# Kernel optimization log

Hardware: AMD Instinct MI355X
Metric: run time of the kernel (lower is better)

The kernel has to match this reference:

```python
import jax, jax.numpy as jnp
import numpy as np

D_MODEL = 1024
N_HEADS = 16
D_K = D_MODEL // N_HEADS


def setup_inputs() -> dict:
    key = jax.random.key(0)
    ks = jax.random.split(key, 5)
    scale = 1.0 / np.sqrt(D_MODEL)
    return {
        "x": jax.random.normal(ks[0], (2, 2048, D_MODEL), dtype=jnp.float32),
        "W_q": jax.random.normal(ks[1], (D_MODEL, D_MODEL), dtype=jnp.float32) * scale,
        "W_k": jax.random.normal(ks[2], (D_MODEL, D_MODEL), dtype=jnp.float32) * scale,
        "W_v": jax.random.normal(ks[3], (D_MODEL, D_MODEL), dtype=jnp.float32) * scale,
        "W_o": jax.random.normal(ks[4], (D_MODEL, D_MODEL), dtype=jnp.float32) * scale,
    }


def reference(x, W_q, W_k, W_v, W_o):
    # Weights are nn.Linear-style [out, in]; Linear(x) = x @ W.T
    B, T, _ = x.shape
    def split_heads(t):  # [B,T,D] -> [B,H,T,d_k]
        return t.reshape(B, T, N_HEADS, D_K).transpose(0, 2, 1, 3)
    Q = split_heads(x @ W_q.T)
    K = split_heads(x @ W_k.T)
    V = split_heads(x @ W_v.T)
    scores = jnp.einsum("bhqd,bhkd->bhqk", Q, K) / jnp.sqrt(jnp.float32(D_K))
    attn_weights = jax.nn.softmax(scores, axis=-1)
    # dropout is identity in eval mode (deterministic reference)
    out = jnp.einsum("bhqk,bhkd->bhqd", attn_weights, V)
    out = out.transpose(0, 2, 1, 3).reshape(B, T, D_MODEL)
    return (out @ W_o.T, attn_weights)
```

## Files before the change

### kernel.cpp

```cpp
#include <hip/hip_runtime.h>
#include <math.h>

#define BB 2
#define TT 2048
#define DM 1024
#define NH 16
#define DKK 64
#define MTOT (BB*TT)
#define BHN (BB*NH)

typedef short bf16x8 __attribute__((ext_vector_type(8)));
typedef float f32x4 __attribute__((ext_vector_type(4)));

static __device__ __forceinline__ unsigned short f32_bf16(float f) {
    union { float f; unsigned u; } v; v.f = f;
    unsigned u = v.u + 0x7fffu + ((v.u >> 16) & 1u);
    return (unsigned short)(u >> 16);
}
static __device__ __forceinline__ float bf16_f32(unsigned short h) {
    union { unsigned u; float f; } v; v.u = (unsigned)h << 16;
    return v.f;
}
static __device__ __forceinline__ void split4(float4 v, ushort4* h, ushort4* l) {
    h->x = f32_bf16(v.x); l->x = f32_bf16(v.x - bf16_f32(h->x));
    h->y = f32_bf16(v.y); l->y = f32_bf16(v.y - bf16_f32(h->y));
    h->z = f32_bf16(v.z); l->z = f32_bf16(v.z - bf16_f32(h->z));
    h->w = f32_bf16(v.w); l->w = f32_bf16(v.w - bf16_f32(h->w));
}
static __device__ __forceinline__ void split8(const float* a, bf16x8* h, bf16x8* l) {
#pragma unroll
    for (int e = 0; e < 8; ++e) {
        unsigned short hi = f32_bf16(a[e]);
        (*h)[e] = (short)hi;
        (*l)[e] = (short)f32_bf16(a[e] - bf16_f32(hi));
    }
}

static __device__ __forceinline__ const float* aptr(const float* A, int mode, int m, int k) {
    if (mode != 1) return A + (size_t)m * 1024 + k;
    int b = m >> 11, t = m & 2047;
    int h = k >> 6, d = k & 63;
    return A + (((size_t)(b * 16 + h)) * 2048 + t) * 64 + d;
}

__global__ __launch_bounds__(256) void gemm_bt_x3(
    const float* __restrict__ A, const float* __restrict__ Bt,
    float* __restrict__ C, int mode)
{
    __shared__ __align__(16) unsigned short Ah[128*32];
    __shared__ __align__(16) unsigned short Al[128*32];
    __shared__ __align__(16) unsigned short Bh[128*32];
    __shared__ __align__(16) unsigned short Bl[128*32];

    const int tid = threadIdx.x;
    const int m_base = blockIdx.x * 128;
    const int n_base = blockIdx.y * 128;
    const int lane = tid & 63;
    const int wave = tid >> 6;
    const int wr = wave >> 1, wc = wave & 1;
    const int l16 = lane & 15, lk = lane >> 4;

    f32x4 zero = {0.f, 0.f, 0.f, 0.f};
    f32x4 acc[4][4];
#pragma unroll
    for (int i = 0; i < 4; ++i)
#pragma unroll
        for (int j = 0; j < 4; ++j) acc[i][j] = zero;

    float4 ga[4], gb[4];
#pragma unroll
    for (int q = 0; q < 4; ++q) {
        int fq = tid + q * 256;
        int row = fq >> 3, kq = fq & 7;
        ga[q] = *(const float4*)aptr(A, mode, m_base + row, kq * 4);
        gb[q] = *(const float4*)(Bt + (size_t)(n_base + row) * 1024 + kq * 4);
    }

    for (int ks = 0; ks < 32; ++ks) {
        __syncthreads();
#pragma unroll
        for (int q = 0; q < 4; ++q) {
            int fq = tid + q * 256;
            int row = fq >> 3, kq = fq & 7;
            int sw = (kq >> 1) ^ ((row >> 1) & 3);
            int base = row * 32 + sw * 8 + (kq & 1) * 4;
            ushort4 h, l;
            split4(ga[q], &h, &l);
            *(ushort4*)&Ah[base] = h;
            *(ushort4*)&Al[base] = l;
            split4(gb[q], &h, &l);
            *(ushort4*)&Bh[base] = h;
            *(ushort4*)&Bl[base] = l;
        }
        __syncthreads();

        if (ks + 1 < 32) {
            int k0 = (ks + 1) * 32;
#pragma unroll
            for (int q = 0; q < 4; ++q) {
                int fq = tid + q * 256;
                int row = fq >> 3, kq = fq & 7;
                ga[q] = *(const float4*)aptr(A, mode, m_base + row, k0 + kq * 4);
                gb[q] = *(const float4*)(Bt + (size_t)(n_base + row) * 1024 + k0 + kq * 4);
            }
        }

        bf16x8 fah[4], fal[4], fbh[4], fbl[4];
#pragma unroll
        for (int i = 0; i < 4; ++i) {
            int am = wr * 64 + i * 16 + l16;
            int ao = am * 32 + ((lk ^ ((am >> 1) & 3)) * 8);
            fah[i] = *(const bf16x8*)&Ah[ao];
            fal[i] = *(const bf16x8*)&Al[ao];
            int bn = wc * 64 + i * 16 + l16;
            int bo = bn * 32 + ((lk ^ ((bn >> 1) & 3)) * 8);
            fbh[i] = *(const bf16x8*)&Bh[bo];
            fbl[i] = *(const bf16x8*)&Bl[bo];
        }
#pragma unroll
        for (int i = 0; i < 4; ++i)
#pragma unroll
            for (int j = 0; j < 4; ++j) {
                acc[i][j] = __builtin_amdgcn_mfma_f32_16x16x32_bf16(fah[i], fbh[j], acc[i][j], 0, 0, 0);
                acc[i][j] = __builtin_amdgcn_mfma_f32_16x16x32_bf16(fah[i], fbl[j], acc[i][j], 0, 0, 0);
                acc[i][j] = __builtin_amdgcn_mfma_f32_16x16x32_bf16(fal[i], fbh[j], acc[i][j], 0, 0, 0);
            }
    }

#pragma unroll
    for (int i = 0; i < 4; ++i) {
#pragma unroll
        for (int j = 0; j < 4; ++j) {
            int gn = n_base + wc * 64 + j * 16 + l16;
#pragma unroll
            for (int r = 0; r < 4; ++r) {
                int gm = m_base + wr * 64 + i * 16 + lk * 4 + r;
                float val = acc[i][j][r];
                if (mode == 0) {
                    int b = gm >> 11, t = gm & 2047;
                    int h = gn >> 6, d = gn & 63;
                    C[(((size_t)(b * 16 + h)) * 2048 + t) * 64 + d] = val;
                } else if (mode == 2) {
                    int b = gm >> 11, t = gm & 2047;
                    int h = gn >> 6, d = gn & 63;
                    C[(((size_t)(b * 16 + h)) * 64 + d) * 2048 + t] = val;
                } else {
                    C[(size_t)gm * 1024 + gn] = val;
                }
            }
        }
    }
}

__global__ __launch_bounds__(256) void rowstats(
    const float* __restrict__ Q, const float* __restrict__ Kmat,
    float* __restrict__ rowmax, float* __restrict__ rowsum)
{
    __shared__ __align__(16) unsigned short Kh[64*64];
    __shared__ __align__(16) unsigned short Kl[64*64];

    const int qt = blockIdx.x, bh = blockIdx.y;
    const int tid = threadIdx.x;
    const int lane = tid & 63, wave = tid >> 6;
    const int l16 = lane & 15, lk = lane >> 4;

    const float* Qrow = Q + ((size_t)(bh * 2048 + qt * 64 + wave * 16 + l16)) * 64;
    bf16x8 qh[2], ql[2];
#pragma unroll
    for (int c = 0; c < 2; ++c) {
        float a[8];
        *(float4*)(a)     = *(const float4*)(Qrow + c * 32 + lk * 8);
        *(float4*)(a + 4) = *(const float4*)(Qrow + c * 32 + lk * 8 + 4);
        split8(a, &qh[c], &ql[c]);
    }

    const float* Kb = Kmat + (size_t)bh * 2048 * 64;

    float mrow[4], lrow[4];
#pragma unroll
    for (int r = 0; r < 4; ++r) { mrow[r] = -INFINITY; lrow[r] = 0.0f; }

    for (int kt = 0; kt < 32; ++kt) {
        __syncthreads();
#pragma unroll
        for (int l = 0; l < 4; ++l) {
            int idx = tid + l * 256;
            int col = idx >> 4, d0 = (idx & 15) * 4;
            float4 v = *(const float4*)(Kb + ((size_t)(kt * 64 + col)) * 64 + d0);
            ushort4 h, lo;
            split4(v, &h, &lo);
            int byte = (col * 128 + d0 * 2) ^ ((col & 7) << 4);
            *(ushort4*)((char*)Kh + byte) = h;
            *(ushort4*)((char*)Kl + byte) = lo;
        }
        __syncthreads();

        f32x4 s[4];
#pragma unroll
        for (int j = 0; j < 4; ++j) {
            s[j] = (f32x4){0.f, 0.f, 0.f, 0.f};
            int col = j * 16 + l16;
#pragma unroll
            for (int c = 0; c < 2; ++c) {
                int byte = (col * 128 + c * 64 + lk * 16) ^ ((col & 7) << 4);
                bf16x8 kh = *(const bf16x8*)((const char*)Kh + byte);
                bf16x8 kl = *(const bf16x8*)((const char*)Kl + byte);
                s[j] = __builtin_amdgcn_mfma_f32_16x16x32_bf16(qh[c], kh, s[j], 0, 0, 0);
                s[j] = __builtin_amdgcn_mfma_f32_16x16x32_bf16(qh[c], kl, s[j], 0, 0, 0);
                s[j] = __builtin_amdgcn_mfma_f32_16x16x32_bf16(ql[c], kh, s[j], 0, 0, 0);
            }
        }

#pragma unroll
        for (int r = 0; r < 4; ++r) {
            float sc[4];
#pragma unroll
            for (int j = 0; j < 4; ++j) sc[j] = s[j][r] * 0.125f;
            float mx = fmaxf(fmaxf(sc[0], sc[1]), fmaxf(sc[2], sc[3]));
            float mnew = fmaxf(mrow[r], mx);
            float ls = __expf(sc[0] - mnew) + __expf(sc[1] - mnew)
                     + __expf(sc[2] - mnew) + __expf(sc[3] - mnew);
            lrow[r] = lrow[r] * __expf(mrow[r] - mnew) + ls;
            mrow[r] = mnew;
        }
    }

#pragma unroll
    for (int off = 1; off < 16; off <<= 1) {
#pragma unroll
        for (int r = 0; r < 4; ++r) {
            float mo = __shfl_xor(mrow[r], off);
            float lo = __shfl_xor(lrow[r], off);
            float mn = fmaxf(mrow[r], mo);
            lrow[r] = lrow[r] * __expf(mrow[r] - mn) + lo * __expf(mo - mn);
            mrow[r] = mn;
        }
    }
    if (l16 == 0) {
#pragma unroll
        for (int r = 0; r < 4; ++r) {
            int row = qt * 64 + wave * 16 + lk * 4 + r;
            rowmax[(size_t)bh * 2048 + row] = mrow[r];
            rowsum[(size_t)bh * 2048 + row] = lrow[r];
        }
    }
}

__global__ __launch_bounds__(256) void attn_pv(
    const float* __restrict__ Q, const float* __restrict__ Kmat,
    const float* __restrict__ VT,
    const float* __restrict__ rowmax, const float* __restrict__ rowsum,
    float* __restrict__ wout, float* __restrict__ aout)
{
    __shared__ __align__(16) unsigned short Kh[64*64];
    __shared__ __align__(16) unsigned short Kl[64*64];
    __shared__ __align__(16) unsigned short Vh[64*64];
    __shared__ __align__(16) unsigned short Vl[64*64];
    __shared__ __align__(16) float Ps[64*64];

    const int qt = blockIdx.x, bh = blockIdx.y;
    const int tid = threadIdx.x;
    const int lane = tid & 63, wave = tid >> 6;
    const int l16 = lane & 15, lk = lane >> 4;

    const float* Qrow = Q + ((size_t)(bh * 2048 + qt * 64 + wave * 16 + l16)) * 64;
    bf16x8 qh[2], ql[2];
#pragma unroll
    for (int c = 0; c < 2; ++c) {
        float a[8];
        *(float4*)(a)     = *(const float4*)(Qrow + c * 32 + lk * 8);
        *(float4*)(a + 4) = *(const float4*)(Qrow + c * 32 + lk * 8 + 4);
        split8(a, &qh[c], &ql[c]);
    }

    const float* Kb = Kmat + (size_t)bh * 2048 * 64;
    const float* Vb = VT + (size_t)bh * 64 * 2048;

    float M[4], Li[4];
#pragma unroll
    for (int r = 0; r < 4; ++r) {
        int row = qt * 64 + wave * 16 + lk * 4 + r;
        M[r]  = rowmax[(size_t)bh * 2048 + row];
        Li[r] = 1.0f / rowsum[(size_t)bh * 2048 + row];
    }

    f32x4 accO[4];
#pragma unroll
    for (int j = 0; j < 4; ++j) accO[j] = (f32x4){0.f, 0.f, 0.f, 0.f};

    for (int kt = 0; kt < 32; ++kt) {
        __syncthreads();
#pragma unroll
        for (int l = 0; l < 4; ++l) {
            int idx = tid + l * 256;
            int col = idx >> 4, d0 = (idx & 15) * 4;
            float4 v = *(const float4*)(Kb + ((size_t)(kt * 64 + col)) * 64 + d0);
            ushort4 h, lo;
            split4(v, &h, &lo);
            int byte = (col * 128 + d0 * 2) ^ ((col & 7) << 4);
            *(ushort4*)((char*)Kh + byte) = h;
            *(ushort4*)((char*)Kl + byte) = lo;
        }
#pragma unroll
        for (int l = 0; l < 4; ++l) {
            int idx = tid + l * 256;
            int d = idx >> 4, kq = idx & 15;
            float4 v = *(const float4*)(Vb + (size_t)d * 2048 + kt * 64 + kq * 4);
            ushort4 h, lo;
            split4(v, &h, &lo);
            int byte = (d * 128 + kq * 8) ^ ((d & 7) << 4);
            *(ushort4*)((char*)Vh + byte) = h;
            *(ushort4*)((char*)Vl + byte) = lo;
        }
        __syncthreads();

        f32x4 s[4];
#pragma unroll
        for (int j = 0; j < 4; ++j) {
            s[j] = (f32x4){0.f, 0.f, 0.f, 0.f};
            int col = j * 16 + l16;
#pragma unroll
            for (int c = 0; c < 2; ++c) {
                int byte = (col * 128 + c * 64 + lk * 16) ^ ((col & 7) << 4);
                bf16x8 kh = *(const bf16x8*)((const char*)Kh + byte);
                bf16x8 kl = *(const bf16x8*)((const char*)Kl + byte);
                s[j] = __builtin_amdgcn_mfma_f32_16x16x32_bf16(qh[c], kh, s[j], 0, 0, 0);
                s[j] = __builtin_amdgcn_mfma_f32_16x16x32_bf16(qh[c], kl, s[j], 0, 0, 0);
                s[j] = __builtin_amdgcn_mfma_f32_16x16x32_bf16(ql[c], kh, s[j], 0, 0, 0);
            }
        }

#pragma unroll
        for (int j = 0; j < 4; ++j) {
            int col = j * 16 + l16;
#pragma unroll
            for (int r = 0; r < 4; ++r) {
                int qrow = wave * 16 + lk * 4 + r;
                float w = __expf(s[j][r] * 0.125f - M[r]) * Li[r];
                int byte = (qrow * 256 + col * 4) ^ ((qrow & 7) << 4);
                *(float*)((char*)Ps + byte) = w;
            }
        }
        __syncthreads();

        size_t wbase = ((size_t)bh * 2048 + qt * 64) * 2048 + (size_t)kt * 64;
#pragma unroll
        for (int l = 0; l < 4; ++l) {
            int idx = tid + l * 256;
            int q = idx >> 4, kq = idx & 15;
            int byte = (q * 256 + kq * 16) ^ ((q & 7) << 4);
            float4 v = *(const float4*)((const char*)Ps + byte);
            *(float4*)(wout + wbase + (size_t)q * 2048 + kq * 4) = v;
        }

#pragma unroll
        for (int c = 0; c < 2; ++c) {
            int qrow = wave * 16 + l16;
            int b0 = qrow * 256 + c * 128 + lk * 32;
            int swz = (qrow & 7) << 4;
            float p[8];
            *(float4*)(p)     = *(const float4*)((const char*)Ps + (b0 ^ swz));
            *(float4*)(p + 4) = *(const float4*)((const char*)Ps + ((b0 + 16) ^ swz));
            bf16x8 pah, pal;
            split8(p, &pah, &pal);
#pragma unroll
            for (int j = 0; j < 4; ++j) {
                int d = j * 16 + l16;
                int byte = (d * 128 + c * 64 + lk * 16) ^ ((d & 7) << 4);
                bf16x8 vh = *(const bf16x8*)((const char*)Vh + byte);
                bf16x8 vl = *(const bf16x8*)((const char*)Vl + byte);
                accO[j] = __builtin_amdgcn_mfma_f32_16x16x32_bf16(pah, vh, accO[j], 0, 0, 0);
                accO[j] = __builtin_amdgcn_mfma_f32_16x16x32_bf16(pah, vl, accO[j], 0, 0, 0);
                accO[j] = __builtin_amdgcn_mfma_f32_16x16x32_bf16(pal, vh, accO[j], 0, 0, 0);
            }
        }
    }

#pragma unroll
    for (int j = 0; j < 4; ++j) {
        int d = j * 16 + l16;
#pragma unroll
        for (int r = 0; r < 4; ++r) {
            int row = qt * 64 + wave * 16 + lk * 4 + r;
            aout[((size_t)bh * 2048 + row) * 64 + d] = accO[j][r];
        }
    }
}

extern "C" void kernel_launch(void* const* d_in, const int* in_sizes, int n_in,
                              void* d_out, int out_size, void* d_ws, size_t ws_size,
                              hipStream_t stream) {
    const float* x  = (const float*)d_in[0];
    const float* Wq = (const float*)d_in[1];
    const float* Wk = (const float*)d_in[2];
    const float* Wv = (const float*)d_in[3];
    const float* Wo = (const float*)d_in[4];

    float* out0 = (float*)d_out;
    float* out1 = out0 + (size_t)MTOT * DM;

    float* ws   = (float*)d_ws;
    float* Qm   = ws;
    float* Km   = Qm + (size_t)4194304;
    float* VT   = Km + (size_t)4194304;
    float* AO   = VT + (size_t)4194304;
    float* rmax = AO + (size_t)4194304;
    float* rsum = rmax + (size_t)65536;

    dim3 blk(256);
    dim3 gg(32, 8);
    gemm_bt_x3<<<gg, blk, 0, stream>>>(x, Wq, Qm, 0);
    gemm_bt_x3<<<gg, blk, 0, stream>>>(x, Wk, Km, 0);
    gemm_bt_x3<<<gg, blk, 0, stream>>>(x, Wv, VT, 2);

    dim3 ga(32, 32);
    rowstats<<<ga, blk, 0, stream>>>(Qm, Km, rmax, rsum);
    attn_pv<<<ga, blk, 0, stream>>>(Qm, Km, VT, rmax, rsum, out1, AO);

    gemm_bt_x3<<<gg, blk, 0, stream>>>(AO, Wo, out0, 1);
}
```

Baseline: 1.130 ms.

## Prefetch K/V tiles into registers, raise MFMA priority, make P writeback wave-local

Loads the next K (and V) tile from global memory into registers while the current tile computes, so global-load latency overlaps the MFMA work in both attention passes. Wraps the MFMA blocks in s_setprio to favour matrix issue across waves. In the PV pass, each wave now writes only its own 16 rows of attention weights after an lgkmcnt wait rather than a block barrier, and uses nontemporal stores for the large weights output. This costs extra registers for the prefetch buffers, which may lower occupancy.

```diff
diff --git a/kernel.cpp b/kernel.cpp
--- a/kernel.cpp
+++ b/kernel.cpp
@@ -117,6 +117,7 @@
             fbh[i] = *(const bf16x8*)&Bh[bo];
             fbl[i] = *(const bf16x8*)&Bl[bo];
         }
+        __builtin_amdgcn_s_setprio(1);
 #pragma unroll
         for (int i = 0; i < 4; ++i)
 #pragma unroll
@@ -125,6 +126,7 @@
                 acc[i][j] = __builtin_amdgcn_mfma_f32_16x16x32_bf16(fah[i], fbl[j], acc[i][j], 0, 0, 0);
                 acc[i][j] = __builtin_amdgcn_mfma_f32_16x16x32_bf16(fal[i], fbh[j], acc[i][j], 0, 0, 0);
             }
+        __builtin_amdgcn_s_setprio(0);
     }
 
 #pragma unroll
@@ -180,22 +182,39 @@
 #pragma unroll
     for (int r = 0; r < 4; ++r) { mrow[r] = -INFINITY; lrow[r] = 0.0f; }
 
+    float4 pk[4];
+#pragma unroll
+    for (int l = 0; l < 4; ++l) {
+        int idx = tid + l * 256;
+        int col = idx >> 4, d0 = (idx & 15) * 4;
+        pk[l] = *(const float4*)(Kb + (size_t)col * 64 + d0);
+    }
+
     for (int kt = 0; kt < 32; ++kt) {
         __syncthreads();
 #pragma unroll
         for (int l = 0; l < 4; ++l) {
             int idx = tid + l * 256;
             int col = idx >> 4, d0 = (idx & 15) * 4;
-            float4 v = *(const float4*)(Kb + ((size_t)(kt * 64 + col)) * 64 + d0);
             ushort4 h, lo;
-            split4(v, &h, &lo);
+            split4(pk[l], &h, &lo);
             int byte = (col * 128 + d0 * 2) ^ ((col & 7) << 4);
             *(ushort4*)((char*)Kh + byte) = h;
             *(ushort4*)((char*)Kl + byte) = lo;
         }
         __syncthreads();
 
+        if (kt + 1 < 32) {
+#pragma unroll
+            for (int l = 0; l < 4; ++l) {
+                int idx = tid + l * 256;
+                int col = idx >> 4, d0 = (idx & 15) * 4;
+                pk[l] = *(const float4*)(Kb + ((size_t)((kt + 1) * 64 + col)) * 64 + d0);
+            }
+        }
+
         f32x4 s[4];
+        __builtin_amdgcn_s_setprio(1);
 #pragma unroll
         for (int j = 0; j < 4; ++j) {
             s[j] = (f32x4){0.f, 0.f, 0.f, 0.f};
@@ -210,6 +229,7 @@
                 s[j] = __builtin_amdgcn_mfma_f32_16x16x32_bf16(ql[c], kh, s[j], 0, 0, 0);
             }
         }
+        __builtin_amdgcn_s_setprio(0);
 
 #pragma unroll
         for (int r = 0; r < 4; ++r) {
@@ -288,15 +308,23 @@
 #pragma unroll
     for (int j = 0; j < 4; ++j) accO[j] = (f32x4){0.f, 0.f, 0.f, 0.f};
 
+    float4 pk[4], pv[4];
+#pragma unroll
+    for (int l = 0; l < 4; ++l) {
+        int idx = tid + l * 256;
+        int col = idx >> 4, d0 = (idx & 15) * 4;
+        pk[l] = *(const float4*)(Kb + (size_t)col * 64 + d0);
+        pv[l] = *(const float4*)(Vb + (size_t)col * 2048 + (idx & 15) * 4);
+    }
+
     for (int kt = 0; kt < 32; ++kt) {
         __syncthreads();
 #pragma unroll
         for (int l = 0; l < 4; ++l) {
             int idx = tid + l * 256;
             int col = idx >> 4, d0 = (idx & 15) * 4;
-            float4 v = *(const float4*)(Kb + ((size_t)(kt * 64 + col)) * 64 + d0);
             ushort4 h, lo;
-            split4(v, &h, &lo);
+            split4(pk[l], &h, &lo);
             int byte = (col * 128 + d0 * 2) ^ ((col & 7) << 4);
             *(ushort4*)((char*)Kh + byte) = h;
             *(ushort4*)((char*)Kl + byte) = lo;
@@ -305,16 +333,26 @@
         for (int l = 0; l < 4; ++l) {
             int idx = tid + l * 256;
             int d = idx >> 4, kq = idx & 15;
-            float4 v = *(const float4*)(Vb + (size_t)d * 2048 + kt * 64 + kq * 4);
             ushort4 h, lo;
-            split4(v, &h, &lo);
+            split4(pv[l], &h, &lo);
             int byte = (d * 128 + kq * 8) ^ ((d & 7) << 4);
             *(ushort4*)((char*)Vh + byte) = h;
             *(ushort4*)((char*)Vl + byte) = lo;
         }
         __syncthreads();
 
+        if (kt + 1 < 32) {
+#pragma unroll
+            for (int l = 0; l < 4; ++l) {
+                int idx = tid + l * 256;
+                int col = idx >> 4, d0 = (idx & 15) * 4;
+                pk[l] = *(const float4*)(Kb + ((size_t)((kt + 1) * 64 + col)) * 64 + d0);
+                pv[l] = *(const float4*)(Vb + (size_t)col * 2048 + (kt + 1) * 64 + (idx & 15) * 4);
+            }
+        }
+
         f32x4 s[4];
+        __builtin_amdgcn_s_setprio(1);
 #pragma unroll
         for (int j = 0; j < 4; ++j) {
             s[j] = (f32x4){0.f, 0.f, 0.f, 0.f};
@@ -329,6 +367,7 @@
                 s[j] = __builtin_amdgcn_mfma_f32_16x16x32_bf16(ql[c], kh, s[j], 0, 0, 0);
             }
         }
+        __builtin_amdgcn_s_setprio(0);
 
 #pragma unroll
         for (int j = 0; j < 4; ++j) {
@@ -341,18 +380,23 @@
                 *(float*)((char*)Ps + byte) = w;
             }
         }
-        __syncthreads();
-
-        size_t wbase = ((size_t)bh * 2048 + qt * 64) * 2048 + (size_t)kt * 64;
-#pragma unroll
-        for (int l = 0; l < 4; ++l) {
-            int idx = tid + l * 256;
-            int q = idx >> 4, kq = idx & 15;
-            int byte = (q * 256 + kq * 16) ^ ((q & 7) << 4);
-            float4 v = *(const float4*)((const char*)Ps + byte);
-            *(float4*)(wout + wbase + (size_t)q * 2048 + kq * 4) = v;
-        }
-
+        asm volatile("s_waitcnt lgkmcnt(0)" ::: "memory");
+
+        {
+            size_t wbase = ((size_t)bh * 2048 + qt * 64 + wave * 16) * 2048
+                         + (size_t)kt * 64;
+#pragma unroll
+            for (int l = 0; l < 4; ++l) {
+                int idx = lane + l * 64;
+                int q = idx >> 4, kq = idx & 15;
+                int qrow = wave * 16 + q;
+                int byte = (qrow * 256 + kq * 16) ^ ((qrow & 7) << 4);
+                f32x4 v = *(const f32x4*)((const char*)Ps + byte);
+                __builtin_nontemporal_store(v, (f32x4*)(wout + wbase + (size_t)q * 2048 + kq * 4));
+            }
+        }
+
+        __builtin_amdgcn_s_setprio(1);
 #pragma unroll
         for (int c = 0; c < 2; ++c) {
             int qrow = wave * 16 + l16;
@@ -374,6 +418,7 @@
                 accO[j] = __builtin_amdgcn_mfma_f32_16x16x32_bf16(pal, vh, accO[j], 0, 0, 0);
             }
         }
+        __builtin_amdgcn_s_setprio(0);
     }
 
 #pragma unroll
```

After: 926.3 us. 1.22x faster.
